# Performance work log

Hardware: AMD Instinct MI355X
Metric: run time of the kernel (lower is better)

The kernel has to match this reference:

```python
import jax, jax.numpy as jnp
import numpy as np

B, T, C = 512, 256, 192
HEAD = 64

def setup_inputs() -> dict:
    key = jax.random.key(0)
    ks = jax.random.split(key, 5)
    return {
        "x": jax.random.normal(ks[0], (B, T, C), dtype=jnp.float32),
        "Wk": jax.random.normal(ks[1], (C, HEAD), dtype=jnp.float32) * (C ** -0.5),
        "Wq": jax.random.normal(ks[2], (C, HEAD), dtype=jnp.float32) * (C ** -0.5),
        "Wv": jax.random.normal(ks[3], (C, HEAD), dtype=jnp.float32) * (C ** -0.5),
        "pos_table": jax.random.normal(ks[4], (T, C), dtype=jnp.float32),
    }

def reference(x, Wk, Wq, Wv, pos_table):
    Bx, Tx, Cx = x.shape
    scale = Cx ** -0.5  # note: scales by n_embed, not head_size (faithful to source)
    k = jnp.einsum('btc,ch->bth', x, Wk)
    q = jnp.einsum('btc,ch->bth', x, Wq)
    v = jnp.einsum('btc,ch->bth', x, Wv)
    pe = pos_table[:Tx]                       # [T, C]
    pos_k = pe @ Wk                           # [T, H]
    pos_q = pe @ Wq                           # [T, H]
    bias = pos_k @ pos_q.T                    # [T, T]
    wei = jnp.einsum('bqh,bkh->bqk', q, k) * scale + bias
    causal = jnp.tril(jnp.ones((Tx, Tx), dtype=bool))
    wei = jnp.where(causal, wei, -jnp.inf)
    wei = jax.nn.softmax(wei, axis=-1)
    # dropout is identity in inference mode
    out = jnp.einsum('bqk,bkh->bqh', wei, v)
    return out
```

## Files before the change

kernel.cpp:

```cpp
#include <hip/hip_runtime.h>
#include <hip/hip_bf16.h>

typedef unsigned short u16;
typedef unsigned int u32;
using bf16x8 = __attribute__((ext_vector_type(8))) short;
using f32x4  = __attribute__((ext_vector_type(4))) float;

#define BB 512
#define TT 256
#define CC 192
#define HH 64

__device__ __forceinline__ u16 f2bf(float f) {
    __hip_bfloat16 h = __float2bfloat16(f);
    u16 u; __builtin_memcpy(&u, &h, 2); return u;
}


__global__ void wprep_kernel(const float* __restrict__ Wq,
                             const float* __restrict__ Wk,
                             const float* __restrict__ Wv,
                             u16* __restrict__ W_sw) {
    int gid  = blockIdx.x * 256 + threadIdx.x;
    int fid  = gid >> 6, lane = gid & 63;
    int n3   = fid / 6,  ks   = fid % 6;
    int l15  = lane & 15, quad = lane >> 4;
    const float* W = (n3 < 4) ? Wq : (n3 < 8) ? Wk : Wv;
    const int h = (n3 & 3) * 16 + l15;
    u16* dst = W_sw + (size_t)gid * 8;
    #pragma unroll
    for (int u = 0; u < 8; ++u) {
        int c = ks * 32 + quad * 8 + u;
        dst[u] = f2bf(W[c * HH + h]);
    }
}

__global__ void pos_kernel(const float* __restrict__ Wk,
                           const float* __restrict__ Wq,
                           const float* __restrict__ pe,
                           float* __restrict__ poskT, float* __restrict__ posqT) {
    int t = blockIdx.x * 4 + (threadIdx.x >> 6);
    int h = threadIdx.x & 63;
    float ak = 0.f, aq = 0.f;
    for (int c = 0; c < CC; ++c) {
        float p = pe[t * CC + c];
        ak += p * Wk[c * HH + h];
        aq += p * Wq[c * HH + h];
    }
    poskT[h * TT + t] = ak;
    posqT[h * TT + t] = aq;
}

__global__ void bias_kernel(const float* __restrict__ poskT,
                            const float* __restrict__ posqT,
                            float4* __restrict__ bias_sw) {
    const int i = blockIdx.x >> 4, jt = blockIdx.x & 15;
    if (jt > i) return;
    const int lane = threadIdx.x;
    const int l15 = lane & 15, quad = lane >> 4;
    const int tq = i * 16 + quad * 4;
    const int jc = jt * 16 + l15;
    float s[4] = {0.f, 0.f, 0.f, 0.f};
    for (int h = 0; h < HH; ++h) {
        float pq = posqT[h * TT + jc];
        #pragma unroll
        for (int r = 0; r < 4; ++r)
            s[r] += poskT[h * TT + tq + r] * pq;
    }
    bias_sw[blockIdx.x * 64 + lane] = make_float4(s[0], s[1], s[2], s[3]);
}


#define XP 200
#define VP 264
#define PP 40
#define P_ELEMS 640
#define Q_OFF 12800
#define K_OFF 45568
#define V_OFF 78336
#define LDS_TOTAL 112128

__global__ __launch_bounds__(256, 1)
void fused_kernel(const float* __restrict__ x,
                  const u16* __restrict__ W_sw,
                  const float4* __restrict__ bias_sw,
                  float* __restrict__ out) {
    extern __shared__ __align__(16) char smem[];
    u16* xs   = (u16*)smem;
    u16* Qlds = (u16*)(smem + Q_OFF);
    u16* Klds = (u16*)(smem + K_OFF);
    u16* Vt   = (u16*)(smem + V_OFF);

    const int tid  = threadIdx.x;
    const int w    = tid >> 6;
    const int lane = tid & 63;
    const int l15  = lane & 15;
    const int quad = lane >> 4;
    const int b    = blockIdx.x;

    const bf16x8* Wv8 = (const bf16x8*)W_sw;
    bf16x8 Wf[18];
    #pragma unroll
    for (int mat = 0; mat < 3; ++mat)
        #pragma unroll
        for (int ks = 0; ks < 6; ++ks)
            Wf[mat * 6 + ks] = Wv8[(((mat * 4 + w) * 6) + ks) * 64 + lane];
    __builtin_amdgcn_sched_barrier(0);

    const int hs    = w >> 1;
    const int quadp = (w * 2 + (l15 >> 3)) & 3;
    const int uu    = l15 & 7;

    #pragma unroll 1
    for (int c8 = 0; c8 < 8; ++c8) {
        const float* xb = x + ((size_t)b * TT + c8 * 32) * CC;
        #pragma unroll
        for (int it = 0; it < 6; ++it) {
            const int flat = (it * 256 + tid) * 4;
            const int row = flat / CC, col = flat % CC;
            const float4 v = *(const float4*)(xb + flat);
            uint2 pk;
            pk.x = (u32)f2bf(v.x) | ((u32)f2bf(v.y) << 16);
            pk.y = (u32)f2bf(v.z) | ((u32)f2bf(v.w) << 16);
            *(uint2*)&xs[row * XP + col] = pk;
        }
        __syncthreads();

        f32x4 acc[6];
        #pragma unroll
        for (int i = 0; i < 6; ++i) acc[i] = {0.f, 0.f, 0.f, 0.f};
        #pragma unroll
        for (int ks = 0; ks < 6; ++ks) {
            bf16x8 a[2];
            #pragma unroll
            for (int m = 0; m < 2; ++m)
                a[m] = *(const bf16x8*)&xs[(m * 16 + l15) * XP + ks * 32 + quad * 8];
            #pragma unroll
            for (int m = 0; m < 2; ++m)
                #pragma unroll
                for (int mat = 0; mat < 3; ++mat)
                    acc[m * 3 + mat] = __builtin_amdgcn_mfma_f32_16x16x32_bf16(
                        a[m], Wf[mat * 6 + ks], acc[m * 3 + mat], 0, 0, 0);
        }

        #pragma unroll
        for (int m = 0; m < 2; ++m) {
            const int i_loc = c8 * 2 + m;
            const int base  = (i_loc * 2 + hs) * 512 + (quadp * 16 + quad * 4) * 8 + uu;
            #pragma unroll
            for (int r = 0; r < 4; ++r) {
                Qlds[base + r * 8] = f2bf(acc[m * 3 + 0][r]);
                Klds[base + r * 8] = f2bf(acc[m * 3 + 1][r]);
            }
            #pragma unroll
            for (int r = 0; r < 4; ++r)
                Vt[(w * 16 + l15) * VP + i_loc * 16 + quad * 4 + r]
                    = f2bf(acc[m * 3 + 2][r]);
        }
        __syncthreads();
    }

    u16* Pw = (u16*)smem + w * P_ELEMS;
    const float scale = 0.07216878364870322f;
    const f32x4 zero4 = {0.f, 0.f, 0.f, 0.f};
    const bf16x8* qv = (const bf16x8*)Qlds;
    const bf16x8* kv = (const bf16x8*)Klds;

    #pragma unroll 1
    for (int mt = 0; mt < 4; ++mt) {
        const int i = (mt == 0) ? w : (mt == 1) ? 15 - w : (mt == 2) ? 4 + w : 11 - w;
        const int t0 = 16 * i;
        const int J  = i + 1;
        const int Pq = (J + 1) >> 1;

        const bf16x8 qf0 = qv[(i * 2 + 0) * 64 + lane];
        const bf16x8 qf1 = qv[(i * 2 + 1) * 64 + lane];

        f32x4 o[4];
        float m4[4], l4[4];
        #pragma unroll
        for (int n = 0; n < 4; ++n) o[n] = zero4;
        #pragma unroll
        for (int r = 0; r < 4; ++r) { m4[r] = -1e30f; l4[r] = 0.f; }

        #pragma unroll
        for (int p = 0; p < 8; ++p) {
            if (p < Pq) {
                const int jt0 = 2 * p, jt1 = 2 * p + 1;
                f32x4 sa = zero4, sb;
                {
                    bf16x8 k0 = kv[(jt0 * 2 + 0) * 64 + lane];
                    bf16x8 k1 = kv[(jt0 * 2 + 1) * 64 + lane];
                    sa = __builtin_amdgcn_mfma_f32_16x16x32_bf16(qf0, k0, sa, 0, 0, 0);
                    sa = __builtin_amdgcn_mfma_f32_16x16x32_bf16(qf1, k1, sa, 0, 0, 0);
                    const float4 b4 = bias_sw[(i * 16 + jt0) * 64 + lane];
                    sa[0] = sa[0] * scale + b4.x;
                    sa[1] = sa[1] * scale + b4.y;
                    sa[2] = sa[2] * scale + b4.z;
                    sa[3] = sa[3] * scale + b4.w;
                    if (jt0 == i) {
                        #pragma unroll
                        for (int r = 0; r < 4; ++r)
                            if (l15 > quad * 4 + r) sa[r] = -1e30f;
                    }
                }
                if (jt1 < J) {
                    sb = zero4;
                    bf16x8 k0 = kv[(jt1 * 2 + 0) * 64 + lane];
                    bf16x8 k1 = kv[(jt1 * 2 + 1) * 64 + lane];
                    sb = __builtin_amdgcn_mfma_f32_16x16x32_bf16(qf0, k0, sb, 0, 0, 0);
                    sb = __builtin_amdgcn_mfma_f32_16x16x32_bf16(qf1, k1, sb, 0, 0, 0);
                    const float4 b4 = bias_sw[(i * 16 + jt1) * 64 + lane];
                    sb[0] = sb[0] * scale + b4.x;
                    sb[1] = sb[1] * scale + b4.y;
                    sb[2] = sb[2] * scale + b4.z;
                    sb[3] = sb[3] * scale + b4.w;
                    if (jt1 == i) {
                        #pragma unroll
                        for (int r = 0; r < 4; ++r)
                            if (l15 > quad * 4 + r) sb[r] = -1e30f;
                    }
                } else {
                    sb[0] = -1e30f; sb[1] = -1e30f; sb[2] = -1e30f; sb[3] = -1e30f;
                }
                float t4[4];
                #pragma unroll
                for (int r = 0; r < 4; ++r) t4[r] = fmaxf(sa[r], sb[r]);
                #pragma unroll
                for (int d = 1; d < 16; d <<= 1) {
                    #pragma unroll
                    for (int r = 0; r < 4; ++r) t4[r] = fmaxf(t4[r], __shfl_xor(t4[r], d, 64));
                }
                float al[4];
                #pragma unroll
                for (int r = 0; r < 4; ++r) {
                    float mn = fmaxf(m4[r], t4[r]);
                    al[r] = __expf(m4[r] - mn);
                    m4[r] = mn;
                    l4[r] *= al[r];
                }
                #pragma unroll
                for (int n = 0; n < 4; ++n)
                #pragma unroll
                for (int r = 0; r < 4; ++r) o[n][r] *= al[r];
                #pragma unroll
                for (int r = 0; r < 4; ++r) {
                    float e0 = __expf(sa[r] - m4[r]);
                    float e1 = __expf(sb[r] - m4[r]);
                    l4[r] += e0 + e1;
                    Pw[(quad * 4 + r) * PP + l15]      = f2bf(e0);
                    Pw[(quad * 4 + r) * PP + 16 + l15] = f2bf(e1);
                }
                bf16x8 pa = *(const bf16x8*)&Pw[l15 * PP + quad * 8];
                #pragma unroll
                for (int n = 0; n < 4; ++n) {
                    bf16x8 bv = *(const bf16x8*)&Vt[(n * 16 + l15) * VP + p * 32 + quad * 8];
                    o[n] = __builtin_amdgcn_mfma_f32_16x16x32_bf16(pa, bv, o[n], 0, 0, 0);
                }
            }
        }
        #pragma unroll
        for (int d = 1; d < 16; d <<= 1) {
            #pragma unroll
            for (int r = 0; r < 4; ++r) l4[r] += __shfl_xor(l4[r], d, 64);
        }
        float rl4[4];
        #pragma unroll
        for (int r = 0; r < 4; ++r) rl4[r] = 1.f / l4[r];
        float* ob = out + ((size_t)b * TT + t0) * HH;
        #pragma unroll
        for (int n = 0; n < 4; ++n)
        #pragma unroll
        for (int r = 0; r < 4; ++r)
            ob[(quad * 4 + r) * HH + n * 16 + l15] = o[n][r] * rl4[r];
    }
}

extern "C" void kernel_launch(void* const* d_in, const int* in_sizes, int n_in,
                              void* d_out, int out_size, void* d_ws, size_t ws_size,
                              hipStream_t stream) {
    const float* x  = (const float*)d_in[0];
    const float* Wk = (const float*)d_in[1];
    const float* Wq = (const float*)d_in[2];
    const float* Wv = (const float*)d_in[3];
    const float* pe = (const float*)d_in[4];
    float* out = (float*)d_out;

    float*  poskT  = (float*)d_ws;
    float*  posqT  = poskT + TT * HH;
    float4* biassw = (float4*)(posqT + TT * HH);
    u16*    W_sw   = (u16*)((float*)biassw + TT * TT);

    static bool attr_set = false;
    if (!attr_set) {
        hipFuncSetAttribute(reinterpret_cast<const void*>(fused_kernel),
                            hipFuncAttributeMaxDynamicSharedMemorySize, LDS_TOTAL);
        attr_set = true;
    }

    wprep_kernel<<<18, 256, 0, stream>>>(Wq, Wk, Wv, W_sw);
    pos_kernel<<<TT / 4, 256, 0, stream>>>(Wk, Wq, pe, poskT, posqT);
    bias_kernel<<<256, 64, 0, stream>>>(poskT, posqT, biassw);
    fused_kernel<<<BB, 256, LDS_TOTAL, stream>>>(x, W_sw, biassw, out);
}
```

Baseline: 216.0 us.

## Use 512-thread blocks and double-buffer x staging in fused attention

Doubles the block to 8 waves, so each wave computes one 16-row half of the QKV projection per chunk and two query tiles in attention instead of four. The x chunk is double-buffered in LDS, with the next chunk's global loads issued before the current chunk's MFMAs, which removes one barrier per chunk and overlaps load latency with compute. This costs more LDS (about 125KB) and register pressure at 512 threads, and the P scratch area per wave (w*P_ELEMS for w up to 7) must still fit within the earlier LDS regions.

```diff
diff --git a/kernel.cpp b/kernel.cpp
--- a/kernel.cpp
+++ b/kernel.cpp
@@ -75,24 +75,26 @@
 #define VP 264
 #define PP 40
 #define P_ELEMS 640
-#define Q_OFF 12800
-#define K_OFF 45568
-#define V_OFF 78336
-#define LDS_TOTAL 112128
-
-__global__ __launch_bounds__(256, 1)
+#define XBUF 12800
+#define Q_OFF 25600
+#define K_OFF 58368
+#define V_OFF 91136
+#define LDS_TOTAL 124928
+
+__global__ __launch_bounds__(512, 1)
 void fused_kernel(const float* __restrict__ x,
                   const u16* __restrict__ W_sw,
                   const float4* __restrict__ bias_sw,
                   float* __restrict__ out) {
     extern __shared__ __align__(16) char smem[];
-    u16* xs   = (u16*)smem;
     u16* Qlds = (u16*)(smem + Q_OFF);
     u16* Klds = (u16*)(smem + K_OFF);
     u16* Vt   = (u16*)(smem + V_OFF);
 
     const int tid  = threadIdx.x;
     const int w    = tid >> 6;
+    const int w4   = w & 3;
+    const int mh   = w >> 2;
     const int lane = tid & 63;
     const int l15  = lane & 15;
     const int quad = lane >> 4;
@@ -104,58 +106,80 @@
     for (int mat = 0; mat < 3; ++mat)
         #pragma unroll
         for (int ks = 0; ks < 6; ++ks)
-            Wf[mat * 6 + ks] = Wv8[(((mat * 4 + w) * 6) + ks) * 64 + lane];
-    __builtin_amdgcn_sched_barrier(0);
-
-    const int hs    = w >> 1;
-    const int quadp = (w * 2 + (l15 >> 3)) & 3;
+            Wf[mat * 6 + ks] = Wv8[(((mat * 4 + w4) * 6) + ks) * 64 + lane];
+    #pragma unroll
+    for (int j = 0; j < 18; ++j)
+        asm volatile("" : "+v"(Wf[j]));
+
+    const int hs    = w4 >> 1;
+    const int quadp = (w4 * 2 + (l15 >> 3)) & 3;
     const int uu    = l15 & 7;
+
+    {
+        const float* xb = x + (size_t)b * TT * CC;
+        float4 vv[3];
+        #pragma unroll
+        for (int it = 0; it < 3; ++it)
+            vv[it] = *(const float4*)(xb + (it * 512 + tid) * 4);
+        u16* xs = (u16*)smem;
+        #pragma unroll
+        for (int it = 0; it < 3; ++it) {
+            const int flat = (it * 512 + tid) * 4;
+            const int row = flat / CC, col = flat % CC;
+            uint2 pk;
+            pk.x = (u32)f2bf(vv[it].x) | ((u32)f2bf(vv[it].y) << 16);
+            pk.y = (u32)f2bf(vv[it].z) | ((u32)f2bf(vv[it].w) << 16);
+            *(uint2*)&xs[row * XP + col] = pk;
+        }
+    }
+    __syncthreads();
 
     #pragma unroll 1
     for (int c8 = 0; c8 < 8; ++c8) {
-        const float* xb = x + ((size_t)b * TT + c8 * 32) * CC;
-        #pragma unroll
-        for (int it = 0; it < 6; ++it) {
-            const int flat = (it * 256 + tid) * 4;
-            const int row = flat / CC, col = flat % CC;
-            const float4 v = *(const float4*)(xb + flat);
-            uint2 pk;
-            pk.x = (u32)f2bf(v.x) | ((u32)f2bf(v.y) << 16);
-            pk.y = (u32)f2bf(v.z) | ((u32)f2bf(v.w) << 16);
-            *(uint2*)&xs[row * XP + col] = pk;
-        }
-        __syncthreads();
-
-        f32x4 acc[6];
-        #pragma unroll
-        for (int i = 0; i < 6; ++i) acc[i] = {0.f, 0.f, 0.f, 0.f};
+        const int cur = c8 & 1;
+        float4 vnext[3];
+        if (c8 < 7) {
+            const float* xb = x + ((size_t)b * TT + (c8 + 1) * 32) * CC;
+            #pragma unroll
+            for (int it = 0; it < 3; ++it)
+                vnext[it] = *(const float4*)(xb + (it * 512 + tid) * 4);
+        }
+        const u16* xs = (const u16*)(smem + cur * XBUF);
+        f32x4 acc[3];
+        #pragma unroll
+        for (int i = 0; i < 3; ++i) acc[i] = {0.f, 0.f, 0.f, 0.f};
         #pragma unroll
         for (int ks = 0; ks < 6; ++ks) {
-            bf16x8 a[2];
-            #pragma unroll
-            for (int m = 0; m < 2; ++m)
-                a[m] = *(const bf16x8*)&xs[(m * 16 + l15) * XP + ks * 32 + quad * 8];
-            #pragma unroll
-            for (int m = 0; m < 2; ++m)
-                #pragma unroll
-                for (int mat = 0; mat < 3; ++mat)
-                    acc[m * 3 + mat] = __builtin_amdgcn_mfma_f32_16x16x32_bf16(
-                        a[m], Wf[mat * 6 + ks], acc[m * 3 + mat], 0, 0, 0);
-        }
-
-        #pragma unroll
-        for (int m = 0; m < 2; ++m) {
-            const int i_loc = c8 * 2 + m;
+            const bf16x8 a = *(const bf16x8*)&xs[(mh * 16 + l15) * XP + ks * 32 + quad * 8];
+            #pragma unroll
+            for (int mat = 0; mat < 3; ++mat)
+                acc[mat] = __builtin_amdgcn_mfma_f32_16x16x32_bf16(
+                    a, Wf[mat * 6 + ks], acc[mat], 0, 0, 0);
+        }
+        {
+            const int i_loc = c8 * 2 + mh;
             const int base  = (i_loc * 2 + hs) * 512 + (quadp * 16 + quad * 4) * 8 + uu;
             #pragma unroll
             for (int r = 0; r < 4; ++r) {
-                Qlds[base + r * 8] = f2bf(acc[m * 3 + 0][r]);
-                Klds[base + r * 8] = f2bf(acc[m * 3 + 1][r]);
+                Qlds[base + r * 8] = f2bf(acc[0][r]);
+                Klds[base + r * 8] = f2bf(acc[1][r]);
             }
             #pragma unroll
             for (int r = 0; r < 4; ++r)
-                Vt[(w * 16 + l15) * VP + i_loc * 16 + quad * 4 + r]
-                    = f2bf(acc[m * 3 + 2][r]);
+                Vt[(w4 * 16 + l15) * VP + i_loc * 16 + quad * 4 + r]
+                    = f2bf(acc[2][r]);
+        }
+        if (c8 < 7) {
+            u16* xsn = (u16*)(smem + (1 - cur) * XBUF);
+            #pragma unroll
+            for (int it = 0; it < 3; ++it) {
+                const int flat = (it * 512 + tid) * 4;
+                const int row = flat / CC, col = flat % CC;
+                uint2 pk;
+                pk.x = (u32)f2bf(vnext[it].x) | ((u32)f2bf(vnext[it].y) << 16);
+                pk.y = (u32)f2bf(vnext[it].z) | ((u32)f2bf(vnext[it].w) << 16);
+                *(uint2*)&xsn[row * XP + col] = pk;
+            }
         }
         __syncthreads();
     }
@@ -167,8 +191,8 @@
     const bf16x8* kv = (const bf16x8*)Klds;
 
     #pragma unroll 1
-    for (int mt = 0; mt < 4; ++mt) {
-        const int i = (mt == 0) ? w : (mt == 1) ? 15 - w : (mt == 2) ? 4 + w : 11 - w;
+    for (int mt = 0; mt < 2; ++mt) {
+        const int i  = mt ? 15 - w : w;
         const int t0 = 16 * i;
         const int J  = i + 1;
         const int Pq = (J + 1) >> 1;
@@ -301,5 +325,5 @@
     wprep_kernel<<<18, 256, 0, stream>>>(Wq, Wk, Wv, W_sw);
     pos_kernel<<<TT / 4, 256, 0, stream>>>(Wk, Wq, pe, poskT, posqT);
     bias_kernel<<<256, 64, 0, stream>>>(poskT, posqT, biassw);
-    fused_kernel<<<BB, 256, LDS_TOTAL, stream>>>(x, W_sw, biassw, out);
-}
+    fused_kernel<<<BB, 512, LDS_TOTAL, stream>>>(x, W_sw, biassw, out);
+}
```

Measured after the change: 201.1 us. -6.9%, faster.
